# Kernel optimization log

Measured on AMD Instinct MI355X. Metric: run time of the kernel, lower is better.

The kernel has to match this reference:

```python
import jax, jax.numpy as jnp
import numpy as np

B, D, E, K, NC, NH = 8192, 1280, 4, 2, 20, 4
CD = D // NC      # chunk_dim = 64
HD = CD // NH     # head_dim = 16
FF = CD * 4       # ffn hidden = 256
EPS = 1e-8


def setup_inputs() -> dict:
    key = jax.random.key(0)
    ks = jax.random.split(key, 12)
    f = lambda k, sh, s=0.02: jax.random.normal(k, sh, jnp.float32) * s
    return {
        "x": jax.random.normal(ks[0], (B, D), jnp.float32),
        "gate_w1": f(ks[1], (E * 4, D)), "gate_b1": jnp.zeros((E * 4,), jnp.float32),
        "gate_w2": f(ks[2], (E, E * 4)), "gate_b2": jnp.zeros((E,), jnp.float32),
        "pos_embed": f(ks[3], (E, NC, CD)),
        "norm1_g": jnp.ones((E, CD), jnp.float32),
        "in_proj_w": f(ks[4], (E, 3 * CD, CD)), "in_proj_b": jnp.zeros((E, 3 * CD), jnp.float32),
        "out_proj_w": f(ks[5], (E, CD, CD)), "out_proj_b": jnp.zeros((E, CD), jnp.float32),
        "ls1_g": jnp.full((E, CD), 1e-4, jnp.float32),
        "norm2_g": jnp.ones((E, CD), jnp.float32),
        "ffn_w1": f(ks[6], (E, FF, CD)), "ffn_b1": jnp.zeros((E, FF), jnp.float32),
        "ffn_w2": f(ks[7], (E, CD, FF)), "ffn_b2": jnp.zeros((E, CD), jnp.float32),
        "ls2_g": jnp.full((E, CD), 1e-4, jnp.float32),
        "proj_w": f(ks[8], (E, D, D)), "proj_b": jnp.zeros((E, D), jnp.float32),
    }


def _rms(v, g):
    # torch RMSNorm in source: x / (||x||_2 * dim^-0.5 + eps) * g
    n = jnp.linalg.norm(v, axis=-1, keepdims=True) * (CD ** -0.5)
    return v / (n + EPS) * g


def _expert(x, pos, n1g, ipw, ipb, opw, opb, l1, n2g, fw1, fb1, fw2, fb2, l2, pw, pb):
    b = x.shape[0]
    xs = x.reshape(b, NC, CD) + pos            # [b, NC, CD]
    xn = _rms(xs, n1g)
    qkv = xn @ ipw.T + ipb                      # [b, NC, 3*CD]
    q, k, v = jnp.split(qkv, 3, axis=-1)
    q = q.reshape(b, NC, NH, HD).transpose(0, 2, 1, 3)
    k = k.reshape(b, NC, NH, HD).transpose(0, 2, 1, 3)
    v = v.reshape(b, NC, NH, HD).transpose(0, 2, 1, 3)
    att = jax.nn.softmax(jnp.einsum('bhqd,bhkd->bhqk', q, k) * (HD ** -0.5), axis=-1)
    o = jnp.einsum('bhqk,bhkd->bhqd', att, v).transpose(0, 2, 1, 3).reshape(b, NC, CD)
    o = o @ opw.T + opb
    xs = xs + l1 * o                            # residual + LayerScale
    h = jax.nn.relu(_rms(xs, n2g) @ fw1.T + fb1) @ fw2.T + fb2
    xs = xs + l2 * h
    return xs.reshape(b, D) @ pw.T + pb         # final proj [b, D]


def reference(x, gate_w1, gate_b1, gate_w2, gate_b2, pos_embed, norm1_g,
              in_proj_w, in_proj_b, out_proj_w, out_proj_b, ls1_g, norm2_g,
              ffn_w1, ffn_b1, ffn_w2, ffn_b2, ls2_g, proj_w, proj_b):
    logits = jnp.tanh(x @ gate_w1.T + gate_b1) @ gate_w2.T + gate_b2   # [B, E]
    scores = jax.nn.softmax(logits, axis=-1)
    tk_s, tk_i = jax.lax.top_k(scores, K)
    tk_s = tk_s / (tk_s.sum(-1, keepdims=True) + 1e-6)
    onehot = jax.nn.one_hot(tk_i, E, dtype=x.dtype)                    # [B, K, E]
    w = (onehot * tk_s[..., None]).sum(1)                              # [B, E] combine weights
    eout = jax.vmap(_expert, in_axes=(None,) + (0,) * 15)(
        x, pos_embed, norm1_g, in_proj_w, in_proj_b, out_proj_w, out_proj_b,
        ls1_g, norm2_g, ffn_w1, ffn_b1, ffn_w2, ffn_b2, ls2_g, proj_w, proj_b)  # [E, B, D]
    output = jnp.einsum('ebd,be->bd', eout, w)
    aux_loss = jnp.float32(0.0)  # eval mode
    load = onehot.sum((0, 1))    # [E]
    return output, aux_loss, load
```

## Files before the change

### kernel.cpp

```cpp
#include <hip/hip_runtime.h>
#include <hip/hip_bf16.h>
#include <math.h>

#define B_SZ 8192
#define D_SZ 1280
#define NE   4
#define NC   20
#define CD   64
#define NH   4
#define HD   16
#define FF   256

typedef __attribute__((ext_vector_type(8))) short bf16x8;
typedef __attribute__((ext_vector_type(4))) float f32x4;

#define WFENCE() do { asm volatile("s_waitcnt lgkmcnt(0)" ::: "memory"); \
                      __builtin_amdgcn_sched_barrier(0); } while (0)

#define WS_TOPI   256
#define WS_TOPW   (WS_TOPI + 2*B_SZ*4)
#define WS_IDX    (WS_TOPW + 2*B_SZ*4)
#define WS_WGT    (WS_IDX  + 2*B_SZ*4)
#define WS_ER0    (WS_WGT  + 2*B_SZ*4)
#define WS_ER1    (WS_ER0  + B_SZ*4)
#define WS_PRK    (WS_ER1  + B_SZ*4)
#define WS_BBE    (WS_PRK  + B_SZ*4)
#define WS_BBP    (WS_BBE  + 32*4*4)
#define WS_PRA    (WS_BBP  + 32*16*4)
#define WS_PRB    (WS_PRA  + (B_SZ+128)*4)
#define WS_PW1    (WS_PRB  + (B_SZ+128)*4)
#define WS_PW2    (WS_PW1  + (B_SZ+128)*4)
#define WS_PRW    (WS_PW2  + (B_SZ+128)*4)
#define WS_XSF    532480
#define XSF_ROWS  (2*B_SZ + 128)
#define WS_PWB    (WS_XSF + (size_t)XSF_ROWS * D_SZ * 2)
#define WS_IPWB   (WS_PWB  + (size_t)NE * D_SZ * D_SZ * 2)
#define WS_OPWB   (WS_IPWB + (size_t)NE * 192 * 64 * 2)
#define WS_FW1B   (WS_OPWB + (size_t)NE * 64 * 64 * 2)
#define WS_FW2B   (WS_FW1B + (size_t)NE * 256 * 64 * 2)

__global__ __launch_bounds__(256) void convert_pw(const float* __restrict__ pw,
                                                  __hip_bfloat16* __restrict__ pwb)
{
    size_t i = ((size_t)blockIdx.x * 256 + threadIdx.x) * 8;
    float4 a = *(const float4*)(pw + i);
    float4 b = *(const float4*)(pw + i + 4);
    __hip_bfloat16 h[8];
    h[0] = __float2bfloat16(a.x); h[1] = __float2bfloat16(a.y);
    h[2] = __float2bfloat16(a.z); h[3] = __float2bfloat16(a.w);
    h[4] = __float2bfloat16(b.x); h[5] = __float2bfloat16(b.y);
    h[6] = __float2bfloat16(b.z); h[7] = __float2bfloat16(b.w);
    *(uint4*)(pwb + i) = *(uint4*)h;
}

#define N_IPW (NE*192*64)
#define N_OPW (NE*64*64)
#define N_FW1 (NE*256*64)
#define N_FW2 (NE*64*256)
__global__ __launch_bounds__(256) void convert_small(
    const float* __restrict__ ipw, const float* __restrict__ opw,
    const float* __restrict__ fw1, const float* __restrict__ fw2,
    __hip_bfloat16* __restrict__ ipwb, __hip_bfloat16* __restrict__ opwb,
    __hip_bfloat16* __restrict__ fw1b, __hip_bfloat16* __restrict__ fw2b)
{
    size_t i = ((size_t)blockIdx.x * 256 + threadIdx.x) * 8;
    const float* src; __hip_bfloat16* dst; size_t off;
    if (i < N_IPW)                       { src = ipw; dst = ipwb; off = i; }
    else if (i < N_IPW + N_OPW)          { src = opw; dst = opwb; off = i - N_IPW; }
    else if (i < N_IPW + N_OPW + N_FW1)  { src = fw1; dst = fw1b; off = i - N_IPW - N_OPW; }
    else                                 { src = fw2; dst = fw2b; off = i - N_IPW - N_OPW - N_FW1; }
    float4 a = *(const float4*)(src + off);
    float4 b = *(const float4*)(src + off + 4);
    __hip_bfloat16 h[8];
    h[0] = __float2bfloat16(a.x); h[1] = __float2bfloat16(a.y);
    h[2] = __float2bfloat16(a.z); h[3] = __float2bfloat16(a.w);
    h[4] = __float2bfloat16(b.x); h[5] = __float2bfloat16(b.y);
    h[6] = __float2bfloat16(b.z); h[7] = __float2bfloat16(b.w);
    *(uint4*)(dst + off) = *(uint4*)h;
}

__global__ __launch_bounds__(64) void gate_kernel(
    const float* __restrict__ x, const float* __restrict__ gw1, const float* __restrict__ gb1,
    const float* __restrict__ gw2, const float* __restrict__ gb2,
    int* __restrict__ topi, float* __restrict__ topw)
{
    const int b = blockIdx.x;
    const int lane = threadIdx.x;
    float acc[16];
#pragma unroll
    for (int j = 0; j < 16; ++j) acc[j] = 0.f;
    const float* xr = x + (size_t)b * D_SZ;
    for (int t = 0; t < NC; ++t) {
        float xv = xr[t * 64 + lane];
#pragma unroll
        for (int j = 0; j < 16; ++j) acc[j] += xv * gw1[j * D_SZ + t * 64 + lane];
    }
#pragma unroll
    for (int j = 0; j < 16; ++j) {
        acc[j] += __shfl_xor(acc[j], 32, 64);
        acc[j] += __shfl_xor(acc[j], 16, 64);
        acc[j] += __shfl_xor(acc[j], 8, 64);
        acc[j] += __shfl_xor(acc[j], 4, 64);
        acc[j] += __shfl_xor(acc[j], 2, 64);
        acc[j] += __shfl_xor(acc[j], 1, 64);
    }
    if (lane == 0) {
        float h[16];
#pragma unroll
        for (int j = 0; j < 16; ++j) h[j] = tanhf(acc[j] + gb1[j]);
        float l[4];
#pragma unroll
        for (int e = 0; e < 4; ++e) {
            float sv = gb2[e];
#pragma unroll
            for (int j = 0; j < 16; ++j) sv += h[j] * gw2[e * 16 + j];
            l[e] = sv;
        }
        float m = fmaxf(fmaxf(l[0], l[1]), fmaxf(l[2], l[3]));
        float p[4];
        float sum = 0.f;
#pragma unroll
        for (int e = 0; e < 4; ++e) { p[e] = expf(l[e] - m); sum += p[e]; }
#pragma unroll
        for (int e = 0; e < 4; ++e) p[e] /= sum;
        int i1 = 0;
#pragma unroll
        for (int e = 1; e < 4; ++e) if (p[e] > p[i1]) i1 = e;
        int i2 = (i1 == 0) ? 1 : 0;
#pragma unroll
        for (int e = 0; e < 4; ++e) if (e != i1 && p[e] > p[i2]) i2 = e;
        float s1 = p[i1], s2 = p[i2];
        float denom = s1 + s2 + 1e-6f;
        topi[b * 2 + 0] = i1;
        topi[b * 2 + 1] = i2;
        topw[b * 2 + 0] = s1 / denom;
        topw[b * 2 + 1] = s2 / denom;
    }
}

__global__ __launch_bounds__(256) void count_kernel(
    const int* __restrict__ topi,
    int* __restrict__ cnt, int* __restrict__ pcnt,
    int* __restrict__ er0, int* __restrict__ er1, int* __restrict__ prk,
    int* __restrict__ bbe, int* __restrict__ bbp)
{
    __shared__ int he[4], hp[16];
    const int t = threadIdx.x;
    const int blk = blockIdx.x;
    const int b = blk * 256 + t;
    if (t < 4) he[t] = 0;
    if (t < 16) hp[t] = 0;
    __syncthreads();
    int e0 = topi[b * 2], e1 = topi[b * 2 + 1];
    er0[b] = atomicAdd(&he[e0], 1);
    er1[b] = atomicAdd(&he[e1], 1);
    prk[b] = atomicAdd(&hp[e0 * 4 + e1], 1);
    __syncthreads();
    if (t < 4)  bbe[blk * 4 + t]  = atomicAdd(&cnt[t], he[t]);
    if (t < 16) bbp[blk * 16 + t] = atomicAdd(&pcnt[t], hp[t]);
}

__global__ void offsets_kernel(const int* __restrict__ cnt, const int* __restrict__ pcnt,
                               int* __restrict__ offA, int* __restrict__ poff,
                               float* __restrict__ load_out)
{
    if (threadIdx.x == 0 && blockIdx.x == 0) {
        int a = 0;
#pragma unroll
        for (int e = 0; e < 4; ++e) { offA[e] = a; a += cnt[e]; }
        offA[4] = a;
        int q = 0;
#pragma unroll
        for (int p = 0; p < 16; ++p) { poff[p] = q; q += pcnt[p]; }
        poff[16] = q;
#pragma unroll
        for (int e = 0; e < 4; ++e) load_out[e] = (float)cnt[e];
    }
}

__global__ __launch_bounds__(256) void fill_kernel(
    const int* __restrict__ topi, const float* __restrict__ topw,
    const int* __restrict__ offA, const int* __restrict__ poff,
    const int* __restrict__ er0, const int* __restrict__ er1, const int* __restrict__ prk,
    const int* __restrict__ bbe, const int* __restrict__ bbp,
    int* __restrict__ idx_list, float* __restrict__ wgt_list,
    int* __restrict__ prA, int* __restrict__ prB,
    float* __restrict__ pw1, float* __restrict__ pw2, int* __restrict__ prow)
{
    const int b = blockIdx.x * 256 + threadIdx.x;
    const int blk = blockIdx.x;
    int e0 = topi[b * 2], e1 = topi[b * 2 + 1];
    float w0 = topw[b * 2], w1 = topw[b * 2 + 1];
    int slot0 = offA[e0] + bbe[blk * 4 + e0] + er0[b];
    int slot1 = offA[e1] + bbe[blk * 4 + e1] + er1[b];
    idx_list[slot0] = b; wgt_list[slot0] = w0;
    idx_list[slot1] = b; wgt_list[slot1] = w1;
    int p = e0 * 4 + e1;
    int pos = poff[p] + bbp[blk * 16 + p] + prk[b];
    prA[pos] = slot0; prB[pos] = slot1;
    pw1[pos] = w0; pw2[pos] = w1; prow[pos] = b;
}

__global__ __launch_bounds__(256, 3) void expert_inner(
    const float* __restrict__ x, const float* __restrict__ pos,
    const float* __restrict__ n1g,
    const __hip_bfloat16* __restrict__ ipwb, const float* __restrict__ ipb,
    const __hip_bfloat16* __restrict__ opwb, const float* __restrict__ opb,
    const float* __restrict__ ls1, const float* __restrict__ n2g,
    const __hip_bfloat16* __restrict__ fw1b, const float* __restrict__ fb1,
    const __hip_bfloat16* __restrict__ fw2b, const float* __restrict__ fb2,
    const float* __restrict__ ls2,
    const int* __restrict__ offA, const int* __restrict__ idx_list,
    const float* __restrict__ wgt_list,
    __hip_bfloat16* __restrict__ xsf)
{
    __shared__ __hip_bfloat16 s_big[4][32][72];
    __shared__ __hip_bfloat16 s_mid[4][32][40];
    __shared__ __hip_bfloat16 s_vt [4][16][40];

    const int t = threadIdx.x;
    const int w = t >> 6;
    const int lane = t & 63;
    const int l15 = lane & 15, lg = lane >> 4;
    const int s = blockIdx.x * 4 + w;
    const int e = (s >= offA[1]) + (s >= offA[2]) + (s >= offA[3]);
    const int b = idx_list[s];
    const float wgt = wgt_list[s];

    __hip_bfloat16 (* const big)[72] = s_big[w];
    __hip_bfloat16 (* const mid)[40] = s_mid[w];
    __hip_bfloat16 (* const vt)[40]  = s_vt[w];

    const float* xg = x + (size_t)b * D_SZ;
    const float* pg = pos + (size_t)e * D_SZ;

    f32x4 xsr[2][4];

    {
        float g1[4];
#pragma unroll
        for (int nt = 0; nt < 4; ++nt) g1[nt] = n1g[e * CD + nt * 16 + l15];
#pragma unroll
        for (int mt = 0; mt < 2; ++mt)
#pragma unroll
            for (int r = 0; r < 4; ++r) {
                const int row = mt * 16 + lg * 4 + r;
                float ss = 0.f;
#pragma unroll
                for (int nt = 0; nt < 4; ++nt) {
                    float v = 0.f;
                    if (row < NC) v = xg[row * 64 + nt * 16 + l15] + pg[row * 64 + nt * 16 + l15];
                    xsr[mt][nt][r] = v;
                    ss += v * v;
                }
                ss += __shfl_xor(ss, 1); ss += __shfl_xor(ss, 2);
                ss += __shfl_xor(ss, 4); ss += __shfl_xor(ss, 8);
                float inv = __builtin_amdgcn_rcpf(sqrtf(ss) * 0.125f + 1e-8f);
#pragma unroll
                for (int nt = 0; nt < 4; ++nt)
                    big[row][nt * 16 + l15] = __float2bfloat16(xsr[mt][nt][r] * inv * g1[nt]);
            }
    }
    WFENCE();

    bf16x8 af[2][2];
#pragma unroll
    for (int mt = 0; mt < 2; ++mt)
#pragma unroll
        for (int ks = 0; ks < 2; ++ks)
            af[mt][ks] = *(const bf16x8*)&big[mt * 16 + l15][ks * 32 + lg * 8];

    for (int h = 0; h < NH; ++h) {
        f32x4 qa[2], ka[2], va[2];
#pragma unroll
        for (int mt = 0; mt < 2; ++mt) { qa[mt] = (f32x4){0,0,0,0}; ka[mt] = (f32x4){0,0,0,0}; va[mt] = (f32x4){0,0,0,0}; }
        const int nq = h * 16 + l15;
#pragma unroll
        for (int ks = 0; ks < 2; ++ks) {
            bf16x8 bq = *(const bf16x8*)(ipwb + ((size_t)(e * 192 + nq)) * 64 + ks * 32 + lg * 8);
            bf16x8 bk_ = *(const bf16x8*)(ipwb + ((size_t)(e * 192 + 64 + nq)) * 64 + ks * 32 + lg * 8);
            bf16x8 bv_ = *(const bf16x8*)(ipwb + ((size_t)(e * 192 + 128 + nq)) * 64 + ks * 32 + lg * 8);
#pragma unroll
            for (int mt = 0; mt < 2; ++mt) {
                qa[mt] = __builtin_amdgcn_mfma_f32_16x16x32_bf16(af[mt][ks], bq, qa[mt], 0, 0, 0);
                ka[mt] = __builtin_amdgcn_mfma_f32_16x16x32_bf16(af[mt][ks], bk_, ka[mt], 0, 0, 0);
                va[mt] = __builtin_amdgcn_mfma_f32_16x16x32_bf16(af[mt][ks], bv_, va[mt], 0, 0, 0);
            }
        }
        const float biq = ipb[e * 192 + nq];
        const float bik = ipb[e * 192 + 64 + nq];
        const float biv = ipb[e * 192 + 128 + nq];
#pragma unroll
        for (int mt = 0; mt < 2; ++mt)
#pragma unroll
            for (int r = 0; r < 4; ++r) {
                const int row = mt * 16 + lg * 4 + r;
                mid[row][l15]      = __float2bfloat16(qa[mt][r] + biq);
                mid[row][16 + l15] = __float2bfloat16(ka[mt][r] + bik);
                vt[l15][row]       = __float2bfloat16(va[mt][r] + biv);
            }
        WFENCE();

        bf16x8 aq[2], bk[2], bv;
        const bf16x8 zf = {0,0,0,0,0,0,0,0};
#pragma unroll
        for (int mt = 0; mt < 2; ++mt) {
            aq[mt] = zf;
            if (lg < 2) aq[mt] = *(const bf16x8*)&mid[mt * 16 + l15][lg * 8];
        }
#pragma unroll
        for (int nt = 0; nt < 2; ++nt) {
            bk[nt] = zf;
            if (lg < 2) bk[nt] = *(const bf16x8*)&mid[nt * 16 + l15][16 + lg * 8];
        }
        bv = *(const bf16x8*)&vt[l15][lg * 8];

        f32x4 sc[2][2];
#pragma unroll
        for (int mt = 0; mt < 2; ++mt)
#pragma unroll
            for (int nt = 0; nt < 2; ++nt)
                sc[mt][nt] = __builtin_amdgcn_mfma_f32_16x16x32_bf16(aq[mt], bk[nt], (f32x4){0,0,0,0}, 0, 0, 0);

#pragma unroll
        for (int mt = 0; mt < 2; ++mt)
#pragma unroll
            for (int r = 0; r < 4; ++r) {
                float e0 = __expf(sc[mt][0][r] * 0.25f);
                float e1 = (l15 < 4) ? __expf(sc[mt][1][r] * 0.25f) : 0.f;
                float sm = e0 + e1;
                sm += __shfl_xor(sm, 1); sm += __shfl_xor(sm, 2);
                sm += __shfl_xor(sm, 4); sm += __shfl_xor(sm, 8);
                float is = __builtin_amdgcn_rcpf(sm);
                const int row = mt * 16 + lg * 4 + r;
                mid[row][l15]      = __float2bfloat16(e0 * is);
                mid[row][16 + l15] = __float2bfloat16((l15 < 4) ? e1 * is : 0.f);
            }
        WFENCE();

#pragma unroll
        for (int mt = 0; mt < 2; ++mt) {
            bf16x8 ap = *(const bf16x8*)&mid[mt * 16 + l15][lg * 8];
            f32x4 o = __builtin_amdgcn_mfma_f32_16x16x32_bf16(ap, bv, (f32x4){0,0,0,0}, 0, 0, 0);
#pragma unroll
            for (int r = 0; r < 4; ++r)
                big[mt * 16 + lg * 4 + r][h * 16 + l15] = __float2bfloat16(o[r]);
        }
        WFENCE();
    }

    {
        bf16x8 aO[2][2];
#pragma unroll
        for (int mt = 0; mt < 2; ++mt)
#pragma unroll
            for (int ks = 0; ks < 2; ++ks)
                aO[mt][ks] = *(const bf16x8*)&big[mt * 16 + l15][ks * 32 + lg * 8];
#pragma unroll
        for (int nt = 0; nt < 4; ++nt) {
            const int n = nt * 16 + l15;
            f32x4 po[2] = {{0,0,0,0},{0,0,0,0}};
#pragma unroll
            for (int ks = 0; ks < 2; ++ks) {
                bf16x8 bw = *(const bf16x8*)(opwb + ((size_t)(e * 64 + n)) * 64 + ks * 32 + lg * 8);
#pragma unroll
                for (int mt = 0; mt < 2; ++mt)
                    po[mt] = __builtin_amdgcn_mfma_f32_16x16x32_bf16(aO[mt][ks], bw, po[mt], 0, 0, 0);
            }
            const float lv = ls1[e * 64 + n], ob = opb[e * 64 + n];
#pragma unroll
            for (int mt = 0; mt < 2; ++mt)
#pragma unroll
                for (int r = 0; r < 4; ++r)
                    xsr[mt][nt][r] += lv * (po[mt][r] + ob);
        }
    }

    {
        float g2[4];
#pragma unroll
        for (int nt = 0; nt < 4; ++nt) g2[nt] = n2g[e * CD + nt * 16 + l15];
#pragma unroll
        for (int mt = 0; mt < 2; ++mt)
#pragma unroll
            for (int r = 0; r < 4; ++r) {
                const int row = mt * 16 + lg * 4 + r;
                float ss = 0.f;
#pragma unroll
                for (int nt = 0; nt < 4; ++nt) ss += xsr[mt][nt][r] * xsr[mt][nt][r];
                ss += __shfl_xor(ss, 1); ss += __shfl_xor(ss, 2);
                ss += __shfl_xor(ss, 4); ss += __shfl_xor(ss, 8);
                float inv = __builtin_amdgcn_rcpf(sqrtf(ss) * 0.125f + 1e-8f);
#pragma unroll
                for (int nt = 0; nt < 4; ++nt)
                    big[row][nt * 16 + l15] = __float2bfloat16(xsr[mt][nt][r] * inv * g2[nt]);
            }
    }
    WFENCE();

    {
        bf16x8 af2[2][2];
#pragma unroll
        for (int mt = 0; mt < 2; ++mt)
#pragma unroll
            for (int ks = 0; ks < 2; ++ks)
                af2[mt][ks] = *(const bf16x8*)&big[mt * 16 + l15][ks * 32 + lg * 8];

        f32x4 a2[2][4];
#pragma unroll
        for (int mt = 0; mt < 2; ++mt)
#pragma unroll
            for (int nt = 0; nt < 4; ++nt) a2[mt][nt] = (f32x4){0,0,0,0};

        for (int c = 0; c < 8; ++c) {
#pragma unroll
            for (int ntc = 0; ntc < 2; ++ntc) {
                const int n = c * 32 + ntc * 16 + l15;
                f32x4 hc[2] = {{0,0,0,0},{0,0,0,0}};
#pragma unroll
                for (int ks = 0; ks < 2; ++ks) {
                    bf16x8 bw = *(const bf16x8*)(fw1b + ((size_t)(e * 256 + n)) * 64 + ks * 32 + lg * 8);
#pragma unroll
                    for (int mt = 0; mt < 2; ++mt)
                        hc[mt] = __builtin_amdgcn_mfma_f32_16x16x32_bf16(af2[mt][ks], bw, hc[mt], 0, 0, 0);
                }
                const float b1 = fb1[e * 256 + n];
#pragma unroll
                for (int mt = 0; mt < 2; ++mt)
#pragma unroll
                    for (int r = 0; r < 4; ++r)
                        mid[mt * 16 + lg * 4 + r][ntc * 16 + l15] =
                            __float2bfloat16(fmaxf(hc[mt][r] + b1, 0.f));
            }
            WFENCE();
            bf16x8 ah[2];
#pragma unroll
            for (int mt = 0; mt < 2; ++mt)
                ah[mt] = *(const bf16x8*)&mid[mt * 16 + l15][lg * 8];
#pragma unroll
            for (int nt = 0; nt < 4; ++nt) {
                const int n = nt * 16 + l15;
                bf16x8 bw2 = *(const bf16x8*)(fw2b + ((size_t)(e * 64 + n)) * 256 + c * 32 + lg * 8);
#pragma unroll
                for (int mt = 0; mt < 2; ++mt)
                    a2[mt][nt] = __builtin_amdgcn_mfma_f32_16x16x32_bf16(ah[mt], bw2, a2[mt][nt], 0, 0, 0);
            }
            WFENCE();
        }

#pragma unroll
        for (int nt = 0; nt < 4; ++nt) {
            const int n = nt * 16 + l15;
            const float lv = ls2[e * 64 + n], b2 = fb2[e * 64 + n];
#pragma unroll
            for (int mt = 0; mt < 2; ++mt)
#pragma unroll
                for (int r = 0; r < 4; ++r)
                    xsr[mt][nt][r] += lv * (a2[mt][nt][r] + b2);
        }
    }

#pragma unroll
    for (int mt = 0; mt < 2; ++mt)
#pragma unroll
        for (int r = 0; r < 4; ++r) {
            const int row = mt * 16 + lg * 4 + r;
            if (row < NC) {
#pragma unroll
                for (int nt = 0; nt < 4; ++nt)
                    xsf[(size_t)s * D_SZ + row * 64 + nt * 16 + l15] =
                        __float2bfloat16(wgt * xsr[mt][nt][r]);
            }
        }
}

#define PROWP 130

__global__ __launch_bounds__(256) void proj_pair(
    const __hip_bfloat16* __restrict__ xsf, const __hip_bfloat16* __restrict__ pwb,
    const float* __restrict__ pb, const int* __restrict__ poff,
    const int* __restrict__ prA, const int* __restrict__ prB,
    const float* __restrict__ pw1, const float* __restrict__ pw2,
    const int* __restrict__ prow, float* __restrict__ out)
{
    __shared__ short As[8][PROWP][8];
    __shared__ short Bs[8][PROWP][8];
    __shared__ int   sSlot[2][128];
    __shared__ float sW[2][128];
    __shared__ int   sRow[128];

    int mblk = blockIdx.x;
    int p = 0, base = 0, M = 0;
#pragma unroll
    for (int pp = 0; pp < 16; ++pp) {
        int b0 = poff[pp], b1 = poff[pp + 1];
        int nb = (b1 - b0 + 127) >> 7;
        if (p == pp && mblk >= nb) { mblk -= nb; p = pp + 1; }
        else if (p == pp) { base = b0; M = b1 - b0; }
    }
    if (p >= 16) return;
    const int ea = p >> 2, eb = p & 3;

    const int m0 = mblk * 128;
    const int n0 = blockIdx.y * 128;
    const int t = threadIdx.x;
    const int w = t >> 6, lane = t & 63;
    const int wm = (w & 1) * 64, wn = (w >> 1) * 64;
    const int l15 = lane & 15, lg = lane >> 4;

    if (t < 128) {
        int posn = base + m0 + t;
        int sa = prA[posn], sb = prB[posn];
        sSlot[0][t] = min(max(sa, 0), 2 * B_SZ);
        sSlot[1][t] = min(max(sb, 0), 2 * B_SZ);
        sW[0][t] = pw1[posn]; sW[1][t] = pw2[posn];
        sRow[t] = prow[posn];
    }
    __syncthreads();

    f32x4 acc[4][4];
#pragma unroll
    for (int i = 0; i < 4; ++i)
#pragma unroll
        for (int j = 0; j < 4; ++j) acc[i][j] = (f32x4){0.f, 0.f, 0.f, 0.f};

    const int arow0 = t >> 3;
    const int akb = t & 7;

#pragma unroll
    for (int ph = 0; ph < 2; ++ph) {
        const __hip_bfloat16* Bg = pwb + (size_t)(ph ? eb : ea) * D_SZ * D_SZ + (size_t)n0 * D_SZ;
        int aslot[4];
#pragma unroll
        for (int i = 0; i < 4; ++i) aslot[i] = sSlot[ph][arow0 + 32 * i];

        for (int kt = 0; kt < D_SZ; kt += 64) {
            __syncthreads();
#pragma unroll
            for (int i = 0; i < 4; ++i) {
                int row = arow0 + 32 * i;
                *(uint4*)&As[akb][row][0] =
                    *(const uint4*)(xsf + (size_t)aslot[i] * D_SZ + kt + akb * 8);
                *(uint4*)&Bs[akb][row][0] =
                    *(const uint4*)(Bg + (size_t)row * D_SZ + kt + akb * 8);
            }
            __syncthreads();
#pragma unroll
            for (int ks = 0; ks < 2; ++ks) {
                int kb = ks * 4 + lg;
                bf16x8 af[4], bfr[4];
#pragma unroll
                for (int ti = 0; ti < 4; ++ti) af[ti]  = *(const bf16x8*)&As[kb][wm + ti * 16 + l15][0];
#pragma unroll
                for (int tj = 0; tj < 4; ++tj) bfr[tj] = *(const bf16x8*)&Bs[kb][wn + tj * 16 + l15][0];
#pragma unroll
                for (int ti = 0; ti < 4; ++ti)
#pragma unroll
                    for (int tj = 0; tj < 4; ++tj)
                        acc[ti][tj] = __builtin_amdgcn_mfma_f32_16x16x32_bf16(
                            af[ti], bfr[tj], acc[ti][tj], 0, 0, 0);
            }
        }
    }

    float pbva[4], pbvb[4];
#pragma unroll
    for (int tj = 0; tj < 4; ++tj) {
        int nc = n0 + wn + tj * 16 + l15;
        pbva[tj] = pb[(size_t)ea * D_SZ + nc];
        pbvb[tj] = pb[(size_t)eb * D_SZ + nc];
    }

#pragma unroll
    for (int ti = 0; ti < 4; ++ti) {
#pragma unroll
        for (int r = 0; r < 4; ++r) {
            int m = wm + ti * 16 + lg * 4 + r;
            if (m0 + m < M) {
                float w1 = sW[0][m], w2 = sW[1][m];
                float* orow = out + (size_t)sRow[m] * D_SZ + n0 + wn + l15;
#pragma unroll
                for (int tj = 0; tj < 4; ++tj)
                    orow[tj * 16] = acc[ti][tj][r] + w1 * pbva[tj] + w2 * pbvb[tj];
            }
        }
    }
}

extern "C" void kernel_launch(void* const* d_in, const int* in_sizes, int n_in,
                              void* d_out, int out_size, void* d_ws, size_t ws_size,
                              hipStream_t stream)
{
    const float* x   = (const float*)d_in[0];
    const float* gw1 = (const float*)d_in[1];
    const float* gb1 = (const float*)d_in[2];
    const float* gw2 = (const float*)d_in[3];
    const float* gb2 = (const float*)d_in[4];
    const float* pos = (const float*)d_in[5];
    const float* n1g = (const float*)d_in[6];
    const float* ipw = (const float*)d_in[7];
    const float* ipb = (const float*)d_in[8];
    const float* opw = (const float*)d_in[9];
    const float* opb = (const float*)d_in[10];
    const float* ls1 = (const float*)d_in[11];
    const float* n2g = (const float*)d_in[12];
    const float* fw1 = (const float*)d_in[13];
    const float* fb1 = (const float*)d_in[14];
    const float* fw2 = (const float*)d_in[15];
    const float* fb2 = (const float*)d_in[16];
    const float* ls2 = (const float*)d_in[17];
    const float* pw  = (const float*)d_in[18];
    const float* pb  = (const float*)d_in[19];

    float* out = (float*)d_out;

    char* ws = (char*)d_ws;
    int*   cnt      = (int*)(ws + 0);
    int*   pcnt     = (int*)(ws + 16);
    int*   offA     = (int*)(ws + 80);
    int*   poff     = (int*)(ws + 112);
    int*   topi     = (int*)(ws + WS_TOPI);
    float* topw     = (float*)(ws + WS_TOPW);
    int*   idx_list = (int*)(ws + WS_IDX);
    float* wgt_list = (float*)(ws + WS_WGT);
    int*   er0      = (int*)(ws + WS_ER0);
    int*   er1      = (int*)(ws + WS_ER1);
    int*   prk      = (int*)(ws + WS_PRK);
    int*   bbe      = (int*)(ws + WS_BBE);
    int*   bbp      = (int*)(ws + WS_BBP);
    int*   prA      = (int*)(ws + WS_PRA);
    int*   prB      = (int*)(ws + WS_PRB);
    float* pw1      = (float*)(ws + WS_PW1);
    float* pw2      = (float*)(ws + WS_PW2);
    int*   prow     = (int*)(ws + WS_PRW);
    __hip_bfloat16* xsf  = (__hip_bfloat16*)(ws + WS_XSF);
    __hip_bfloat16* pwb  = (__hip_bfloat16*)(ws + WS_PWB);
    __hip_bfloat16* ipwb = (__hip_bfloat16*)(ws + WS_IPWB);
    __hip_bfloat16* opwb = (__hip_bfloat16*)(ws + WS_OPWB);
    __hip_bfloat16* fw1b = (__hip_bfloat16*)(ws + WS_FW1B);
    __hip_bfloat16* fw2b = (__hip_bfloat16*)(ws + WS_FW2B);

    hipMemsetAsync(d_ws, 0, 256, stream);
    hipMemsetAsync(out + (size_t)B_SZ * D_SZ, 0, 5 * sizeof(float), stream);

    float* load_out = out + (size_t)B_SZ * D_SZ + 1;

    convert_pw<<<NE * D_SZ * D_SZ / (256 * 8), 256, 0, stream>>>(pw, pwb);
    convert_small<<<(N_IPW + N_OPW + N_FW1 + N_FW2) / (256 * 8), 256, 0, stream>>>(
        ipw, opw, fw1, fw2, ipwb, opwb, fw1b, fw2b);
    gate_kernel<<<B_SZ, 64, 0, stream>>>(x, gw1, gb1, gw2, gb2, topi, topw);
    count_kernel<<<B_SZ / 256, 256, 0, stream>>>(topi, cnt, pcnt, er0, er1, prk, bbe, bbp);
    offsets_kernel<<<1, 64, 0, stream>>>(cnt, pcnt, offA, poff, load_out);
    fill_kernel<<<B_SZ / 256, 256, 0, stream>>>(topi, topw, offA, poff, er0, er1, prk,
                                                bbe, bbp, idx_list, wgt_list,
                                                prA, prB, pw1, pw2, prow);
    expert_inner<<<(2 * B_SZ) / 4, 256, 0, stream>>>(x, pos, n1g, ipwb, ipb, opwb, opb, ls1,
                                                     n2g, fw1b, fb1, fw2b, fb2, ls2,
                                                     offA, idx_list, wgt_list, xsf);
    proj_pair<<<dim3(96, D_SZ / 128), 256, 0, stream>>>(
        xsf, pwb, pb, poff, prA, prB, pw1, pw2, prow, out);
}
```

Measured before the change: 529.2 us.

## Software-pipeline expert weight loads and double-buffer FFN hidden tiles in LDS

Prefetches the next head's QKV weights, the next FFN1 weight chunk and the first out-proj weight tile into registers while the current MFMAs run. The FFN hidden activations now alternate between two LDS buffers so a trailing wait fence per chunk can be dropped, and the head and FFN loops are fully unrolled. Launch bounds are raised from 3 to 4 blocks per CU, which tightens the register budget and risks spills given the extra prefetch registers.

```diff
diff --git a/kernel.cpp b/kernel.cpp
--- a/kernel.cpp
+++ b/kernel.cpp
@@ -201,7 +201,7 @@
     pw1[pos] = w0; pw2[pos] = w1; prow[pos] = b;
 }
 
-__global__ __launch_bounds__(256, 3) void expert_inner(
+__global__ __launch_bounds__(256, 4) void expert_inner(
     const float* __restrict__ x, const float* __restrict__ pos,
     const float* __restrict__ n1g,
     const __hip_bfloat16* __restrict__ ipwb, const float* __restrict__ ipb,
@@ -233,8 +233,35 @@
 
     const float* xg = x + (size_t)b * D_SZ;
     const float* pg = pos + (size_t)e * D_SZ;
+    const __hip_bfloat16* ipw_e = ipwb + (size_t)e * 192 * 64;
+    const float* ipb_e = ipb + e * 192;
 
     f32x4 xsr[2][4];
+
+#pragma unroll
+    for (int mt = 0; mt < 2; ++mt)
+#pragma unroll
+        for (int r = 0; r < 4; ++r) {
+            const int row = mt * 16 + lg * 4 + r;
+#pragma unroll
+            for (int nt = 0; nt < 4; ++nt) {
+                float v = 0.f;
+                if (row < NC) v = xg[row * 64 + nt * 16 + l15] + pg[row * 64 + nt * 16 + l15];
+                xsr[mt][nt][r] = v;
+            }
+        }
+
+    bf16x8 wq[2], wk[2], wv[2];
+    float pbq, pbk, pbv;
+    {
+#pragma unroll
+        for (int ks = 0; ks < 2; ++ks) {
+            wq[ks] = *(const bf16x8*)(ipw_e + (size_t)(l15) * 64 + ks * 32 + lg * 8);
+            wk[ks] = *(const bf16x8*)(ipw_e + (size_t)(64 + l15) * 64 + ks * 32 + lg * 8);
+            wv[ks] = *(const bf16x8*)(ipw_e + (size_t)(128 + l15) * 64 + ks * 32 + lg * 8);
+        }
+        pbq = ipb_e[l15]; pbk = ipb_e[64 + l15]; pbv = ipb_e[128 + l15];
+    }
 
     {
         float g1[4];
@@ -247,12 +274,7 @@
                 const int row = mt * 16 + lg * 4 + r;
                 float ss = 0.f;
 #pragma unroll
-                for (int nt = 0; nt < 4; ++nt) {
-                    float v = 0.f;
-                    if (row < NC) v = xg[row * 64 + nt * 16 + l15] + pg[row * 64 + nt * 16 + l15];
-                    xsr[mt][nt][r] = v;
-                    ss += v * v;
-                }
+                for (int nt = 0; nt < 4; ++nt) ss += xsr[mt][nt][r] * xsr[mt][nt][r];
                 ss += __shfl_xor(ss, 1); ss += __shfl_xor(ss, 2);
                 ss += __shfl_xor(ss, 4); ss += __shfl_xor(ss, 8);
                 float inv = __builtin_amdgcn_rcpf(sqrtf(ss) * 0.125f + 1e-8f);
@@ -270,34 +292,38 @@
         for (int ks = 0; ks < 2; ++ks)
             af[mt][ks] = *(const bf16x8*)&big[mt * 16 + l15][ks * 32 + lg * 8];
 
+#pragma unroll
     for (int h = 0; h < NH; ++h) {
         f32x4 qa[2], ka[2], va[2];
 #pragma unroll
         for (int mt = 0; mt < 2; ++mt) { qa[mt] = (f32x4){0,0,0,0}; ka[mt] = (f32x4){0,0,0,0}; va[mt] = (f32x4){0,0,0,0}; }
-        const int nq = h * 16 + l15;
-#pragma unroll
-        for (int ks = 0; ks < 2; ++ks) {
-            bf16x8 bq = *(const bf16x8*)(ipwb + ((size_t)(e * 192 + nq)) * 64 + ks * 32 + lg * 8);
-            bf16x8 bk_ = *(const bf16x8*)(ipwb + ((size_t)(e * 192 + 64 + nq)) * 64 + ks * 32 + lg * 8);
-            bf16x8 bv_ = *(const bf16x8*)(ipwb + ((size_t)(e * 192 + 128 + nq)) * 64 + ks * 32 + lg * 8);
+#pragma unroll
+        for (int ks = 0; ks < 2; ++ks)
 #pragma unroll
             for (int mt = 0; mt < 2; ++mt) {
-                qa[mt] = __builtin_amdgcn_mfma_f32_16x16x32_bf16(af[mt][ks], bq, qa[mt], 0, 0, 0);
-                ka[mt] = __builtin_amdgcn_mfma_f32_16x16x32_bf16(af[mt][ks], bk_, ka[mt], 0, 0, 0);
-                va[mt] = __builtin_amdgcn_mfma_f32_16x16x32_bf16(af[mt][ks], bv_, va[mt], 0, 0, 0);
-            }
-        }
-        const float biq = ipb[e * 192 + nq];
-        const float bik = ipb[e * 192 + 64 + nq];
-        const float biv = ipb[e * 192 + 128 + nq];
+                qa[mt] = __builtin_amdgcn_mfma_f32_16x16x32_bf16(af[mt][ks], wq[ks], qa[mt], 0, 0, 0);
+                ka[mt] = __builtin_amdgcn_mfma_f32_16x16x32_bf16(af[mt][ks], wk[ks], ka[mt], 0, 0, 0);
+                va[mt] = __builtin_amdgcn_mfma_f32_16x16x32_bf16(af[mt][ks], wv[ks], va[mt], 0, 0, 0);
+            }
+        const float cbq = pbq, cbk = pbk, cbv = pbv;
+        if (h < NH - 1) {
+            const int nqn = (h + 1) * 16 + l15;
+#pragma unroll
+            for (int ks = 0; ks < 2; ++ks) {
+                wq[ks] = *(const bf16x8*)(ipw_e + (size_t)(nqn) * 64 + ks * 32 + lg * 8);
+                wk[ks] = *(const bf16x8*)(ipw_e + (size_t)(64 + nqn) * 64 + ks * 32 + lg * 8);
+                wv[ks] = *(const bf16x8*)(ipw_e + (size_t)(128 + nqn) * 64 + ks * 32 + lg * 8);
+            }
+            pbq = ipb_e[nqn]; pbk = ipb_e[64 + nqn]; pbv = ipb_e[128 + nqn];
+        }
 #pragma unroll
         for (int mt = 0; mt < 2; ++mt)
 #pragma unroll
             for (int r = 0; r < 4; ++r) {
                 const int row = mt * 16 + lg * 4 + r;
-                mid[row][l15]      = __float2bfloat16(qa[mt][r] + biq);
-                mid[row][16 + l15] = __float2bfloat16(ka[mt][r] + bik);
-                vt[l15][row]       = __float2bfloat16(va[mt][r] + biv);
+                mid[row][l15]      = __float2bfloat16(qa[mt][r] + cbq);
+                mid[row][16 + l15] = __float2bfloat16(ka[mt][r] + cbk);
+                vt[l15][row]       = __float2bfloat16(va[mt][r] + cbv);
             }
         WFENCE();
 
@@ -346,8 +372,14 @@
             for (int r = 0; r < 4; ++r)
                 big[mt * 16 + lg * 4 + r][h * 16 + l15] = __float2bfloat16(o[r]);
         }
-        WFENCE();
-    }
+    }
+
+    const __hip_bfloat16* opw_e = opwb + (size_t)e * 64 * 64;
+    bf16x8 ow0[2];
+#pragma unroll
+    for (int ks = 0; ks < 2; ++ks)
+        ow0[ks] = *(const bf16x8*)(opw_e + (size_t)(l15) * 64 + ks * 32 + lg * 8);
+    WFENCE();
 
     {
         bf16x8 aO[2][2];
@@ -362,7 +394,8 @@
             f32x4 po[2] = {{0,0,0,0},{0,0,0,0}};
 #pragma unroll
             for (int ks = 0; ks < 2; ++ks) {
-                bf16x8 bw = *(const bf16x8*)(opwb + ((size_t)(e * 64 + n)) * 64 + ks * 32 + lg * 8);
+                bf16x8 bw = (nt == 0) ? ow0[ks]
+                          : *(const bf16x8*)(opw_e + (size_t)n * 64 + ks * 32 + lg * 8);
 #pragma unroll
                 for (int mt = 0; mt < 2; ++mt)
                     po[mt] = __builtin_amdgcn_mfma_f32_16x16x32_bf16(aO[mt][ks], bw, po[mt], 0, 0, 0);
@@ -396,6 +429,17 @@
                     big[row][nt * 16 + l15] = __float2bfloat16(xsr[mt][nt][r] * inv * g2[nt]);
             }
     }
+
+    const __hip_bfloat16* f1_e = fw1b + (size_t)e * 256 * 64;
+    const float* fb1_e = fb1 + e * 256;
+    bf16x8 f1a[2], f1b[2];
+    float pb1a, pb1b;
+#pragma unroll
+    for (int ks = 0; ks < 2; ++ks) {
+        f1a[ks] = *(const bf16x8*)(f1_e + (size_t)(l15) * 64 + ks * 32 + lg * 8);
+        f1b[ks] = *(const bf16x8*)(f1_e + (size_t)(16 + l15) * 64 + ks * 32 + lg * 8);
+    }
+    pb1a = fb1_e[l15]; pb1b = fb1_e[16 + l15];
     WFENCE();
 
     {
@@ -412,40 +456,66 @@
 #pragma unroll
             for (int nt = 0; nt < 4; ++nt) a2[mt][nt] = (f32x4){0,0,0,0};
 
+        const __hip_bfloat16* f2_e = fw2b + (size_t)e * 64 * 256;
+
+#pragma unroll
         for (int c = 0; c < 8; ++c) {
-#pragma unroll
-            for (int ntc = 0; ntc < 2; ++ntc) {
-                const int n = c * 32 + ntc * 16 + l15;
-                f32x4 hc[2] = {{0,0,0,0},{0,0,0,0}};
+            f32x4 h0[2] = {{0,0,0,0},{0,0,0,0}};
+            f32x4 h1[2] = {{0,0,0,0},{0,0,0,0}};
+#pragma unroll
+            for (int ks = 0; ks < 2; ++ks)
+#pragma unroll
+                for (int mt = 0; mt < 2; ++mt) {
+                    h0[mt] = __builtin_amdgcn_mfma_f32_16x16x32_bf16(af2[mt][ks], f1a[ks], h0[mt], 0, 0, 0);
+                    h1[mt] = __builtin_amdgcn_mfma_f32_16x16x32_bf16(af2[mt][ks], f1b[ks], h1[mt], 0, 0, 0);
+                }
+            const float cb1a = pb1a, cb1b = pb1b;
+            if (c < 7) {
+                const int n0 = (c + 1) * 32 + l15;
 #pragma unroll
                 for (int ks = 0; ks < 2; ++ks) {
-                    bf16x8 bw = *(const bf16x8*)(fw1b + ((size_t)(e * 256 + n)) * 64 + ks * 32 + lg * 8);
-#pragma unroll
-                    for (int mt = 0; mt < 2; ++mt)
-                        hc[mt] = __builtin_amdgcn_mfma_f32_16x16x32_bf16(af2[mt][ks], bw, hc[mt], 0, 0, 0);
+                    f1a[ks] = *(const bf16x8*)(f1_e + (size_t)(n0) * 64 + ks * 32 + lg * 8);
+                    f1b[ks] = *(const bf16x8*)(f1_e + (size_t)(n0 + 16) * 64 + ks * 32 + lg * 8);
                 }
-                const float b1 = fb1[e * 256 + n];
+                pb1a = fb1_e[n0]; pb1b = fb1_e[n0 + 16];
+            }
+            if (c & 1) {
 #pragma unroll
                 for (int mt = 0; mt < 2; ++mt)
 #pragma unroll
-                    for (int r = 0; r < 4; ++r)
-                        mid[mt * 16 + lg * 4 + r][ntc * 16 + l15] =
-                            __float2bfloat16(fmaxf(hc[mt][r] + b1, 0.f));
+                    for (int r = 0; r < 4; ++r) {
+                        const int row = mt * 16 + lg * 4 + r;
+                        big[row][l15]      = __float2bfloat16(fmaxf(h0[mt][r] + cb1a, 0.f));
+                        big[row][16 + l15] = __float2bfloat16(fmaxf(h1[mt][r] + cb1b, 0.f));
+                    }
+            } else {
+#pragma unroll
+                for (int mt = 0; mt < 2; ++mt)
+#pragma unroll
+                    for (int r = 0; r < 4; ++r) {
+                        const int row = mt * 16 + lg * 4 + r;
+                        mid[row][l15]      = __float2bfloat16(fmaxf(h0[mt][r] + cb1a, 0.f));
+                        mid[row][16 + l15] = __float2bfloat16(fmaxf(h1[mt][r] + cb1b, 0.f));
+                    }
             }
             WFENCE();
             bf16x8 ah[2];
-#pragma unroll
-            for (int mt = 0; mt < 2; ++mt)
-                ah[mt] = *(const bf16x8*)&mid[mt * 16 + l15][lg * 8];
+            if (c & 1) {
+#pragma unroll
+                for (int mt = 0; mt < 2; ++mt)
+                    ah[mt] = *(const bf16x8*)&big[mt * 16 + l15][lg * 8];
+            } else {
+#pragma unroll
+                for (int mt = 0; mt < 2; ++mt)
+                    ah[mt] = *(const bf16x8*)&mid[mt * 16 + l15][lg * 8];
+            }
 #pragma unroll
             for (int nt = 0; nt < 4; ++nt) {
-                const int n = nt * 16 + l15;
-                bf16x8 bw2 = *(const bf16x8*)(fw2b + ((size_t)(e * 64 + n)) * 256 + c * 32 + lg * 8);
+                bf16x8 w2 = *(const bf16x8*)(f2_e + (size_t)(nt * 16 + l15) * 256 + c * 32 + lg * 8);
 #pragma unroll
                 for (int mt = 0; mt < 2; ++mt)
-                    a2[mt][nt] = __builtin_amdgcn_mfma_f32_16x16x32_bf16(ah[mt], bw2, a2[mt][nt], 0, 0, 0);
-            }
-            WFENCE();
+                    a2[mt][nt] = __builtin_amdgcn_mfma_f32_16x16x32_bf16(ah[mt], w2, a2[mt][nt], 0, 0, 0);
+            }
         }
 
 #pragma unroll
```

After: 527.2 us. No clear change (-0.4%).

## Shrink LDS in expert_inner, transpose V via bpermute, vectorize xsf stores

Applied to the files above, without the earlier changes.

Drops the per-wave `mid` and `vt` shared buffers and reuses the single `big` tile for Q/K, softmax probabilities and the FFN hidden chunk, ping-ponging between two column halves. The V transpose now uses `ds_bpermute` on packed bf16 registers instead of going through LDS. Attention outputs are held in packed registers until all heads finish. The explicit waitcnt/sched barriers are removed and min occupancy is raised from 3 to 5 waves. The aim is more resident waves and fewer LDS round-trips, and the final xsf writes are staged through LDS as 16-byte stores. Without the manual fences, correctness depends on the compiler inserting the right LDS waits, and the higher occupancy target may cause register spills.

```diff
diff --git a/kernel.cpp b/kernel.cpp
--- a/kernel.cpp
+++ b/kernel.cpp
@@ -14,8 +14,14 @@
 typedef __attribute__((ext_vector_type(8))) short bf16x8;
 typedef __attribute__((ext_vector_type(4))) float f32x4;
 
-#define WFENCE() do { asm volatile("s_waitcnt lgkmcnt(0)" ::: "memory"); \
-                      __builtin_amdgcn_sched_barrier(0); } while (0)
+__device__ inline unsigned int pk2(float lo, float hi) {
+    union { __hip_bfloat16 h; unsigned short s; } a, b;
+    a.h = __float2bfloat16(lo); b.h = __float2bfloat16(hi);
+    return (unsigned int)a.s | ((unsigned int)b.s << 16);
+}
+__device__ inline __hip_bfloat16 us2bf(unsigned short u) {
+    union { unsigned short s; __hip_bfloat16 h; } c; c.s = u; return c.h;
+}
 
 #define WS_TOPI   256
 #define WS_TOPW   (WS_TOPI + 2*B_SZ*4)
@@ -201,7 +207,7 @@
     pw1[pos] = w0; pw2[pos] = w1; prow[pos] = b;
 }
 
-__global__ __launch_bounds__(256, 3) void expert_inner(
+__global__ __launch_bounds__(256, 5) void expert_inner(
     const float* __restrict__ x, const float* __restrict__ pos,
     const float* __restrict__ n1g,
     const __hip_bfloat16* __restrict__ ipwb, const float* __restrict__ ipb,
@@ -215,8 +221,6 @@
     __hip_bfloat16* __restrict__ xsf)
 {
     __shared__ __hip_bfloat16 s_big[4][32][72];
-    __shared__ __hip_bfloat16 s_mid[4][32][40];
-    __shared__ __hip_bfloat16 s_vt [4][16][40];
 
     const int t = threadIdx.x;
     const int w = t >> 6;
@@ -228,14 +232,26 @@
     const float wgt = wgt_list[s];
 
     __hip_bfloat16 (* const big)[72] = s_big[w];
-    __hip_bfloat16 (* const mid)[40] = s_mid[w];
-    __hip_bfloat16 (* const vt)[40]  = s_vt[w];
 
     const float* xg = x + (size_t)b * D_SZ;
     const float* pg = pos + (size_t)e * D_SZ;
+    const __hip_bfloat16* ipw_e = ipwb + (size_t)e * 192 * 64;
+    const float* ipb_e = ipb + e * 192;
 
     f32x4 xsr[2][4];
 
+#pragma unroll
+    for (int mt = 0; mt < 2; ++mt)
+#pragma unroll
+        for (int r = 0; r < 4; ++r) {
+            const int row = mt * 16 + lg * 4 + r;
+#pragma unroll
+            for (int nt = 0; nt < 4; ++nt) {
+                float v = 0.f;
+                if (row < NC) v = xg[row * 64 + nt * 16 + l15] + pg[row * 64 + nt * 16 + l15];
+                xsr[mt][nt][r] = v;
+            }
+        }
     {
         float g1[4];
 #pragma unroll
@@ -247,12 +263,7 @@
                 const int row = mt * 16 + lg * 4 + r;
                 float ss = 0.f;
 #pragma unroll
-                for (int nt = 0; nt < 4; ++nt) {
-                    float v = 0.f;
-                    if (row < NC) v = xg[row * 64 + nt * 16 + l15] + pg[row * 64 + nt * 16 + l15];
-                    xsr[mt][nt][r] = v;
-                    ss += v * v;
-                }
+                for (int nt = 0; nt < 4; ++nt) ss += xsr[mt][nt][r] * xsr[mt][nt][r];
                 ss += __shfl_xor(ss, 1); ss += __shfl_xor(ss, 2);
                 ss += __shfl_xor(ss, 4); ss += __shfl_xor(ss, 8);
                 float inv = __builtin_amdgcn_rcpf(sqrtf(ss) * 0.125f + 1e-8f);
@@ -261,7 +272,6 @@
                     big[row][nt * 16 + l15] = __float2bfloat16(xsr[mt][nt][r] * inv * g1[nt]);
             }
     }
-    WFENCE();
 
     bf16x8 af[2][2];
 #pragma unroll
@@ -270,50 +280,72 @@
         for (int ks = 0; ks < 2; ++ks)
             af[mt][ks] = *(const bf16x8*)&big[mt * 16 + l15][ks * 32 + lg * 8];
 
+    unsigned int opk[NH][4];
+#pragma unroll
     for (int h = 0; h < NH; ++h) {
+        const int nq = h * 16 + l15;
         f32x4 qa[2], ka[2], va[2];
 #pragma unroll
         for (int mt = 0; mt < 2; ++mt) { qa[mt] = (f32x4){0,0,0,0}; ka[mt] = (f32x4){0,0,0,0}; va[mt] = (f32x4){0,0,0,0}; }
-        const int nq = h * 16 + l15;
 #pragma unroll
         for (int ks = 0; ks < 2; ++ks) {
-            bf16x8 bq = *(const bf16x8*)(ipwb + ((size_t)(e * 192 + nq)) * 64 + ks * 32 + lg * 8);
-            bf16x8 bk_ = *(const bf16x8*)(ipwb + ((size_t)(e * 192 + 64 + nq)) * 64 + ks * 32 + lg * 8);
-            bf16x8 bv_ = *(const bf16x8*)(ipwb + ((size_t)(e * 192 + 128 + nq)) * 64 + ks * 32 + lg * 8);
+            bf16x8 wq = *(const bf16x8*)(ipw_e + (size_t)(nq) * 64 + ks * 32 + lg * 8);
+            bf16x8 wk = *(const bf16x8*)(ipw_e + (size_t)(64 + nq) * 64 + ks * 32 + lg * 8);
+            bf16x8 wv = *(const bf16x8*)(ipw_e + (size_t)(128 + nq) * 64 + ks * 32 + lg * 8);
 #pragma unroll
             for (int mt = 0; mt < 2; ++mt) {
-                qa[mt] = __builtin_amdgcn_mfma_f32_16x16x32_bf16(af[mt][ks], bq, qa[mt], 0, 0, 0);
-                ka[mt] = __builtin_amdgcn_mfma_f32_16x16x32_bf16(af[mt][ks], bk_, ka[mt], 0, 0, 0);
-                va[mt] = __builtin_amdgcn_mfma_f32_16x16x32_bf16(af[mt][ks], bv_, va[mt], 0, 0, 0);
-            }
-        }
-        const float biq = ipb[e * 192 + nq];
-        const float bik = ipb[e * 192 + 64 + nq];
-        const float biv = ipb[e * 192 + 128 + nq];
+                qa[mt] = __builtin_amdgcn_mfma_f32_16x16x32_bf16(af[mt][ks], wq, qa[mt], 0, 0, 0);
+                ka[mt] = __builtin_amdgcn_mfma_f32_16x16x32_bf16(af[mt][ks], wk, ka[mt], 0, 0, 0);
+                va[mt] = __builtin_amdgcn_mfma_f32_16x16x32_bf16(af[mt][ks], wv, va[mt], 0, 0, 0);
+            }
+        }
+        const float biq = ipb_e[nq], bik = ipb_e[64 + nq], biv = ipb_e[128 + nq];
+
+        unsigned int vp0[2], vp1[2];
+#pragma unroll
+        for (int mt = 0; mt < 2; ++mt) {
+            vp0[mt] = pk2(va[mt][0] + biv, va[mt][1] + biv);
+            vp1[mt] = pk2(va[mt][2] + biv, va[mt][3] + biv);
+        }
+        const int aA = (((lg & 1) * 32) + l15) * 4;
+        const int aB = aA + 64;
+        int d0a = __builtin_amdgcn_ds_bpermute(aA, (int)vp0[0]);
+        int d0b = __builtin_amdgcn_ds_bpermute(aA, (int)vp0[1]);
+        int d1a = __builtin_amdgcn_ds_bpermute(aA, (int)vp1[0]);
+        int d1b = __builtin_amdgcn_ds_bpermute(aA, (int)vp1[1]);
+        int d2a = __builtin_amdgcn_ds_bpermute(aB, (int)vp0[0]);
+        int d2b = __builtin_amdgcn_ds_bpermute(aB, (int)vp0[1]);
+        int d3a = __builtin_amdgcn_ds_bpermute(aB, (int)vp1[0]);
+        int d3b = __builtin_amdgcn_ds_bpermute(aB, (int)vp1[1]);
+        const bool hi2 = (lg >= 2);
+        union { int i[4]; bf16x8 v; } uv;
+        uv.i[0] = hi2 ? d0b : d0a;
+        uv.i[1] = hi2 ? d1b : d1a;
+        uv.i[2] = hi2 ? d2b : d2a;
+        uv.i[3] = hi2 ? d3b : d3a;
+        const bf16x8 bv = uv.v;
+
 #pragma unroll
         for (int mt = 0; mt < 2; ++mt)
 #pragma unroll
             for (int r = 0; r < 4; ++r) {
                 const int row = mt * 16 + lg * 4 + r;
-                mid[row][l15]      = __float2bfloat16(qa[mt][r] + biq);
-                mid[row][16 + l15] = __float2bfloat16(ka[mt][r] + bik);
-                vt[l15][row]       = __float2bfloat16(va[mt][r] + biv);
-            }
-        WFENCE();
-
-        bf16x8 aq[2], bk[2], bv;
+                big[row][l15]      = __float2bfloat16(qa[mt][r] + biq);
+                big[row][16 + l15] = __float2bfloat16(ka[mt][r] + bik);
+            }
+
+        bf16x8 aq[2], bk[2];
         const bf16x8 zf = {0,0,0,0,0,0,0,0};
 #pragma unroll
         for (int mt = 0; mt < 2; ++mt) {
             aq[mt] = zf;
-            if (lg < 2) aq[mt] = *(const bf16x8*)&mid[mt * 16 + l15][lg * 8];
+            if (lg < 2) aq[mt] = *(const bf16x8*)&big[mt * 16 + l15][lg * 8];
         }
 #pragma unroll
         for (int nt = 0; nt < 2; ++nt) {
             bk[nt] = zf;
-            if (lg < 2) bk[nt] = *(const bf16x8*)&mid[nt * 16 + l15][16 + lg * 8];
-        }
-        bv = *(const bf16x8*)&vt[l15][lg * 8];
+            if (lg < 2) bk[nt] = *(const bf16x8*)&big[nt * 16 + l15][16 + lg * 8];
+        }
 
         f32x4 sc[2][2];
 #pragma unroll
@@ -333,22 +365,32 @@
                 sm += __shfl_xor(sm, 4); sm += __shfl_xor(sm, 8);
                 float is = __builtin_amdgcn_rcpf(sm);
                 const int row = mt * 16 + lg * 4 + r;
-                mid[row][l15]      = __float2bfloat16(e0 * is);
-                mid[row][16 + l15] = __float2bfloat16((l15 < 4) ? e1 * is : 0.f);
-            }
-        WFENCE();
+                big[row][l15]      = __float2bfloat16(e0 * is);
+                big[row][16 + l15] = __float2bfloat16((l15 < 4) ? e1 * is : 0.f);
+            }
 
 #pragma unroll
         for (int mt = 0; mt < 2; ++mt) {
-            bf16x8 ap = *(const bf16x8*)&mid[mt * 16 + l15][lg * 8];
+            bf16x8 ap = *(const bf16x8*)&big[mt * 16 + l15][lg * 8];
             f32x4 o = __builtin_amdgcn_mfma_f32_16x16x32_bf16(ap, bv, (f32x4){0,0,0,0}, 0, 0, 0);
-#pragma unroll
-            for (int r = 0; r < 4; ++r)
-                big[mt * 16 + lg * 4 + r][h * 16 + l15] = __float2bfloat16(o[r]);
-        }
-        WFENCE();
-    }
-
+            opk[h][mt * 2 + 0] = pk2(o[0], o[1]);
+            opk[h][mt * 2 + 1] = pk2(o[2], o[3]);
+        }
+    }
+
+#pragma unroll
+    for (int h = 0; h < NH; ++h)
+#pragma unroll
+        for (int mt = 0; mt < 2; ++mt) {
+            const int row0 = mt * 16 + lg * 4;
+            const int col = h * 16 + l15;
+            big[row0 + 0][col] = us2bf((unsigned short)(opk[h][mt * 2 + 0] & 0xffff));
+            big[row0 + 1][col] = us2bf((unsigned short)(opk[h][mt * 2 + 0] >> 16));
+            big[row0 + 2][col] = us2bf((unsigned short)(opk[h][mt * 2 + 1] & 0xffff));
+            big[row0 + 3][col] = us2bf((unsigned short)(opk[h][mt * 2 + 1] >> 16));
+        }
+
+    const __hip_bfloat16* opw_e = opwb + (size_t)e * 64 * 64;
     {
         bf16x8 aO[2][2];
 #pragma unroll
@@ -362,7 +404,7 @@
             f32x4 po[2] = {{0,0,0,0},{0,0,0,0}};
 #pragma unroll
             for (int ks = 0; ks < 2; ++ks) {
-                bf16x8 bw = *(const bf16x8*)(opwb + ((size_t)(e * 64 + n)) * 64 + ks * 32 + lg * 8);
+                bf16x8 bw = *(const bf16x8*)(opw_e + (size_t)n * 64 + ks * 32 + lg * 8);
 #pragma unroll
                 for (int mt = 0; mt < 2; ++mt)
                     po[mt] = __builtin_amdgcn_mfma_f32_16x16x32_bf16(aO[mt][ks], bw, po[mt], 0, 0, 0);
@@ -396,7 +438,6 @@
                     big[row][nt * 16 + l15] = __float2bfloat16(xsr[mt][nt][r] * inv * g2[nt]);
             }
     }
-    WFENCE();
 
     {
         bf16x8 af2[2][2];
@@ -412,40 +453,43 @@
 #pragma unroll
             for (int nt = 0; nt < 4; ++nt) a2[mt][nt] = (f32x4){0,0,0,0};
 
+        const __hip_bfloat16* f1_e = fw1b + (size_t)e * 256 * 64;
+        const float* fb1_e = fb1 + e * 256;
+        const __hip_bfloat16* f2_e = fw2b + (size_t)e * 64 * 256;
+
+#pragma unroll
         for (int c = 0; c < 8; ++c) {
+            const int cb = (c & 1) * 32;
 #pragma unroll
             for (int ntc = 0; ntc < 2; ++ntc) {
                 const int n = c * 32 + ntc * 16 + l15;
                 f32x4 hc[2] = {{0,0,0,0},{0,0,0,0}};
 #pragma unroll
                 for (int ks = 0; ks < 2; ++ks) {
-                    bf16x8 bw = *(const bf16x8*)(fw1b + ((size_t)(e * 256 + n)) * 64 + ks * 32 + lg * 8);
+                    bf16x8 bw = *(const bf16x8*)(f1_e + (size_t)n * 64 + ks * 32 + lg * 8);
 #pragma unroll
                     for (int mt = 0; mt < 2; ++mt)
                         hc[mt] = __builtin_amdgcn_mfma_f32_16x16x32_bf16(af2[mt][ks], bw, hc[mt], 0, 0, 0);
                 }
-                const float b1 = fb1[e * 256 + n];
+                const float b1 = fb1_e[n];
 #pragma unroll
                 for (int mt = 0; mt < 2; ++mt)
 #pragma unroll
                     for (int r = 0; r < 4; ++r)
-                        mid[mt * 16 + lg * 4 + r][ntc * 16 + l15] =
+                        big[mt * 16 + lg * 4 + r][cb + ntc * 16 + l15] =
                             __float2bfloat16(fmaxf(hc[mt][r] + b1, 0.f));
             }
-            WFENCE();
             bf16x8 ah[2];
 #pragma unroll
             for (int mt = 0; mt < 2; ++mt)
-                ah[mt] = *(const bf16x8*)&mid[mt * 16 + l15][lg * 8];
+                ah[mt] = *(const bf16x8*)&big[mt * 16 + l15][cb + lg * 8];
 #pragma unroll
             for (int nt = 0; nt < 4; ++nt) {
-                const int n = nt * 16 + l15;
-                bf16x8 bw2 = *(const bf16x8*)(fw2b + ((size_t)(e * 64 + n)) * 256 + c * 32 + lg * 8);
+                bf16x8 w2 = *(const bf16x8*)(f2_e + (size_t)(nt * 16 + l15) * 256 + c * 32 + lg * 8);
 #pragma unroll
                 for (int mt = 0; mt < 2; ++mt)
-                    a2[mt][nt] = __builtin_amdgcn_mfma_f32_16x16x32_bf16(ah[mt], bw2, a2[mt][nt], 0, 0, 0);
-            }
-            WFENCE();
+                    a2[mt][nt] = __builtin_amdgcn_mfma_f32_16x16x32_bf16(ah[mt], w2, a2[mt][nt], 0, 0, 0);
+            }
         }
 
 #pragma unroll
@@ -468,10 +512,19 @@
             if (row < NC) {
 #pragma unroll
                 for (int nt = 0; nt < 4; ++nt)
-                    xsf[(size_t)s * D_SZ + row * 64 + nt * 16 + l15] =
-                        __float2bfloat16(wgt * xsr[mt][nt][r]);
-            }
-        }
+                    big[row][nt * 16 + l15] = __float2bfloat16(wgt * xsr[mt][nt][r]);
+            }
+        }
+    __hip_bfloat16* xo = xsf + (size_t)s * D_SZ;
+#pragma unroll
+    for (int it = 0; it < 3; ++it) {
+        const int c2 = lane + it * 64;
+        if (c2 < 160) {
+            const int row = c2 >> 3, off = (c2 & 7) * 8;
+            bf16x8 v = *(const bf16x8*)&big[row][off];
+            *(bf16x8*)(xo + row * 64 + off) = v;
+        }
+    }
 }
 
 #define PROWP 130
```

New measurement: 569.7 us. 7.7% more time.
